# Optimization experiments

Measured on AMD Instinct MI355X. Metric: run time of the kernel, lower is better.

Reference implementation:

```python
import jax, jax.numpy as jnp
import numpy as np

N = 50000      # nodes
E = 800000     # edges
T = 3          # npass
ED = 64        # embedding_dim
NS = 23        # nshifts (arange(0.8, 3.0+1e-5, 0.1))
MD = NS + ED   # message_dim = 87
H = 200        # hidden width (hardcoded in module)
NMOL = 2048    # number of molecules (segments for final scatter)
RD = ED * (T + 1)  # readout input dim = 256
EPS = 1e-5

SHIFTS = jnp.asarray(np.arange(0.8, 3.0 + 1e-5, 0.1, dtype=np.float32))  # [23]


def setup_inputs() -> dict:
    key = jax.random.key(0)
    ks = jax.random.split(key, 32)
    inp = {
        'z_i': jax.random.randint(ks[0], (N,), 0, 10),
        'edge_index': jax.random.randint(ks[1], (2, E), 0, N),
        'dist_ij': jax.random.uniform(ks[2], (E, 1), dtype=jnp.float32) * 2.2 + 0.8,
        'mol_ind': jnp.sort(jax.random.randint(ks[3], (N,), 0, NMOL)),
        'emb': jax.random.normal(ks[4], (10, ED), dtype=jnp.float32),
        # per-pass update MLP params, stacked over T
        'up_bn_g': jnp.ones((T, MD), jnp.float32),
        'up_bn_b': jnp.zeros((T, MD), jnp.float32),
        'up_w1': jax.random.normal(ks[5], (T, MD, H), jnp.float32) * 0.05,
        'up_b1': jnp.zeros((T, H), jnp.float32),
        'up_w2': jax.random.normal(ks[6], (T, H, H), jnp.float32) * 0.05,
        'up_b2': jnp.zeros((T, H), jnp.float32),
        'up_w3': jax.random.normal(ks[7], (T, H, H), jnp.float32) * 0.05,
        'up_b3': jnp.zeros((T, H), jnp.float32),
        'up_w4': jax.random.normal(ks[8], (T, H, ED), jnp.float32) * 0.05,
        'up_b4': jnp.zeros((T, ED), jnp.float32),
        # readout MLP params
        'ro_bn_g': jnp.ones((RD,), jnp.float32),
        'ro_bn_b': jnp.zeros((RD,), jnp.float32),
        'ro_w1': jax.random.normal(ks[9], (RD, H), jnp.float32) * 0.05,
        'ro_b1': jnp.zeros((H,), jnp.float32),
        'ro_w2': jax.random.normal(ks[10], (H, H), jnp.float32) * 0.05,
        'ro_b2': jnp.zeros((H,), jnp.float32),
        'ro_w3': jax.random.normal(ks[11], (H, H), jnp.float32) * 0.05,
        'ro_b3': jnp.zeros((H,), jnp.float32),
        'ro_w4': jax.random.normal(ks[12], (H, 1), jnp.float32) * 0.05,
        'ro_b4': jnp.zeros((1,), jnp.float32),  # bias filled to 0 in __init__
    }
    return inp


def batchnorm(x, g, b):
    # BatchNorm1d in training mode: batch statistics, biased variance
    mu = jnp.mean(x, axis=0)
    var = jnp.mean(jnp.square(x - mu), axis=0)
    return (x - mu) * jax.lax.rsqrt(var + EPS) * g + b


def mlp(x, g, b, w1, b1, w2, b2, w3, b3, w4, b4):
    x = batchnorm(x, g, b)
    x = jax.nn.relu(x @ w1 + b1)
    x = jax.nn.relu(x @ w2 + b2)
    x = jax.nn.relu(x @ w3 + b3)
    return x @ w4 + b4


def reference(z_i, edge_index, dist_ij, mol_ind, emb,
              up_bn_g, up_bn_b, up_w1, up_b1, up_w2, up_b2, up_w3, up_b3, up_w4, up_b4,
              ro_bn_g, ro_bn_b, ro_w1, ro_b1, ro_w2, ro_b2, ro_w3, ro_b3, ro_w4, ro_b4):
    e_source, e_sink = edge_index[0], edge_index[1]
    rbf_ij = jnp.exp(-jnp.square(dist_ij - SHIFTS[None, :]))  # [E, NS]
    x_i = emb[z_i]                                            # [N, ED]
    x_list = [x_i]
    for t in range(T):
        m_ij = jnp.concatenate([rbf_ij, x_i[e_sink]], axis=1)  # [E, MD] gather
        m_i = jax.ops.segment_sum(m_ij, e_source, num_segments=N)  # scatter-sum
        x_i = x_i + 0.1 * mlp(m_i, up_bn_g[t], up_bn_b[t],
                              up_w1[t], up_b1[t], up_w2[t], up_b2[t],
                              up_w3[t], up_b3[t], up_w4[t], up_b4[t])
        x_list.append(x_i)
    x_all = jnp.concatenate(x_list, axis=1)  # [N, RD]
    y_i = mlp(x_all, ro_bn_g, ro_bn_b, ro_w1, ro_b1, ro_w2, ro_b2, ro_w3, ro_b3, ro_w4, ro_b4)
    y = jax.ops.segment_sum(y_i, mol_ind, num_segments=NMOL)  # [NMOL, 1]
    return y
```

## Files before the change

kernel.cpp:

```cpp
#include <hip/hip_runtime.h>
#include <hip/hip_bf16.h>
#include <type_traits>

#define NN 50000
#define NP 50048
#define EE 800000
#define TT 3
#define ED 64
#define NS 23
#define MD 87
#define HH 200
#define NMOL 2048
#define RD 256

#define SP 216
#define NPB2 512
#define SNB ((NN + 255) / 256)

typedef __attribute__((ext_vector_type(8))) short short8b;
typedef __attribute__((ext_vector_type(4))) short short4b;
typedef __attribute__((ext_vector_type(4))) float f32x4;

__device__ __forceinline__ unsigned short f2bf(float f) {
  unsigned u = __float_as_uint(f);
  return (unsigned short)((u + 0x7fffu + ((u >> 16) & 1u)) >> 16);
}
__device__ __forceinline__ float ubf2f(unsigned short h) {
  return __uint_as_float(((unsigned)h) << 16);
}
__device__ __forceinline__ float bfp2f(unsigned p) {
  return __uint_as_float(p << 16) + __uint_as_float(p & 0xffff0000u);
}
__device__ __forceinline__ unsigned packsplit(float v) {
  unsigned short h = f2bf(v);
  unsigned short l = f2bf(v - ubf2f(h));
  return (unsigned)h | ((unsigned)l << 16);
}

struct WD { const float* src; short* dst; int K, N, Kpad, Npad, T; };
struct WDs { WD d[5]; };

__global__ __launch_bounds__(256) void wprep_kernel(WDs W) {
  WD w = W.d[blockIdx.y];
  int KB = w.Kpad >> 5, NT = w.Npad >> 4;
  int per = w.Npad * w.Kpad;
  int total = w.T * per;
  for (int idx = blockIdx.x * 256 + threadIdx.x; idx < total; idx += gridDim.x * 256) {
    int t = idx / per;
    int r = idx - t * per;
    int e = r & 7, lane = (r >> 3) & 63;
    int blk = r >> 9;
    int kb = blk % KB, tile = blk / KB;
    int ln = lane & 15, quad = lane >> 4;
    int n = tile * 16 + ln, k = kb * 32 + quad * 8 + e;
    float v = 0.f;
    if (k < w.K && n < w.N) v = w.src[((size_t)t * w.K + k) * w.N + n];
    unsigned short h = f2bf(v);
    unsigned short l = f2bf(v - ubf2f(h));
    size_t base = ((size_t)(t * NT + tile) * KB + kb) * 1024;
    w.dst[base + lane * 8 + e] = (short)h;
    w.dst[base + 512 + lane * 8 + e] = (short)l;
  }
}

__global__ __launch_bounds__(256) void wscale_kernel(const float* __restrict__ wsrc,
                                                     const float* __restrict__ na,
                                                     const float* __restrict__ nb,
                                                     const float* __restrict__ bsrc,
                                                     int K, int Kpad,
                                                     short* __restrict__ wsp,
                                                     float* __restrict__ bc) {
  int n = blockIdx.x;
  int k = threadIdx.x;
  int KB = Kpad >> 5;
  int tile = n >> 4, ln = n & 15;
  float contrib = 0.f;
  if (k < Kpad) {
    float v = 0.f;
    if (n < HH && k < K) {
      float w = wsrc[(size_t)k * HH + n];
      v = na[k] * w;
      contrib = nb[k] * w;
    }
    unsigned short h = f2bf(v);
    unsigned short l = f2bf(v - ubf2f(h));
    int kb = k >> 5, quad = (k & 31) >> 3, e = k & 7;
    int lane = quad * 16 + ln;
    size_t base = ((size_t)tile * KB + kb) * 1024;
    wsp[base + lane * 8 + e] = (short)h;
    wsp[base + 512 + lane * 8 + e] = (short)l;
  }
  __shared__ float sh[256];
  sh[k] = contrib;
  __syncthreads();
  for (int off = 128; off > 0; off >>= 1) {
    if (k < off) sh[k] += sh[k + off];
    __syncthreads();
  }
  if (k == 0) bc[n] = (n < HH ? bsrc[n] : 0.f) + sh[0];
}

__global__ __launch_bounds__(256) void emb_kernel(const int* __restrict__ z,
                                                  const float* __restrict__ emb,
                                                  unsigned* __restrict__ xp,
                                                  short* __restrict__ xq) {
  int idx = blockIdx.x * 256 + threadIdx.x;
  if (idx >= NN * ED) return;
  int i = idx >> 6, d = idx & 63;
  unsigned pk = packsplit(emb[z[i] * ED + d]);
  xp[(size_t)i * RD + d] = pk;
  xq[(size_t)i * RD + d] = (short)(pk & 0xffffu);
}

__global__ __launch_bounds__(256) void hist_kernel(const int* __restrict__ src,
                                                   int* __restrict__ deg) {
  int e = blockIdx.x * 256 + threadIdx.x;
  if (e < EE) atomicAdd(&deg[src[e]], 1);
}

__global__ __launch_bounds__(256) void scanA_kernel(const int* __restrict__ deg,
                                                    int* __restrict__ Psum) {
  int i = blockIdx.x * 256 + threadIdx.x;
  int v = (i < NN) ? deg[i] : 0;
#pragma unroll
  for (int off = 32; off > 0; off >>= 1) v += __shfl_down(v, off, 64);
  __shared__ int ws[4];
  if ((threadIdx.x & 63) == 0) ws[threadIdx.x >> 6] = v;
  __syncthreads();
  if (threadIdx.x == 0) Psum[blockIdx.x] = ws[0] + ws[1] + ws[2] + ws[3];
}

__global__ __launch_bounds__(256) void scanB_kernel(const int* __restrict__ Psum,
                                                    int* __restrict__ Poff) {
  __shared__ int sh[256];
  int t = threadIdx.x;
  int v = (t < SNB) ? Psum[t] : 0;
  sh[t] = v;
  __syncthreads();
  for (int off = 1; off < 256; off <<= 1) {
    int u = (t >= off) ? sh[t - off] : 0;
    __syncthreads();
    sh[t] += u;
    __syncthreads();
  }
  if (t < SNB) Poff[t] = sh[t] - v;
}

__global__ __launch_bounds__(256) void scanC_kernel(const int* __restrict__ deg,
                                                    const int* __restrict__ Poff,
                                                    int* __restrict__ offs,
                                                    int* __restrict__ cursor) {
  __shared__ int sh[256];
  int t = threadIdx.x;
  int i = blockIdx.x * 256 + t;
  int v = (i < NN) ? deg[i] : 0;
  sh[t] = v;
  __syncthreads();
  for (int off = 1; off < 256; off <<= 1) {
    int u = (t >= off) ? sh[t - off] : 0;
    __syncthreads();
    sh[t] += u;
    __syncthreads();
  }
  int excl = Poff[blockIdx.x] + sh[t] - v;
  if (i < NN) {
    offs[i] = excl;
    cursor[i] = excl;
    if (i == NN - 1) offs[NN] = excl + v;
  }
}

__global__ __launch_bounds__(256) void scatter_kernel(const int* __restrict__ src,
                                                      const int* __restrict__ snk,
                                                      const float* __restrict__ dist,
                                                      int* __restrict__ cursor,
                                                      int* __restrict__ ssink,
                                                      float* __restrict__ sdist) {
  int e = blockIdx.x * 256 + threadIdx.x;
  if (e >= EE) return;
  int p = atomicAdd(&cursor[src[e]], 1);
  ssink[p] = snk[e];
  sdist[p] = dist[e];
}

__global__ __launch_bounds__(256) void gather_kernel(const int* __restrict__ offs,
                                                     const int* __restrict__ ssink,
                                                     const float* __restrict__ sdist,
                                                     const short* __restrict__ xq,
                                                     int toff, short* __restrict__ mh) {
  int node = blockIdx.x * 4 + (threadIdx.x >> 6);
  int lane = threadIdx.x & 63;
  if (node >= NN) return;
  float shift = (float)(0.8 + 0.1 * (double)lane);
  int e0 = offs[node], e1 = offs[node + 1];
  float ax0 = 0.f, ax1 = 0.f, ar0 = 0.f, ar1 = 0.f;
  int j = e0;
  for (; j + 4 <= e1; j += 4) {
    int s0 = ssink[j], s1 = ssink[j + 1], s2 = ssink[j + 2], s3 = ssink[j + 3];
    float d0 = sdist[j], d1 = sdist[j + 1], d2 = sdist[j + 2], d3 = sdist[j + 3];
    float x0 = ubf2f((unsigned short)xq[(size_t)s0 * RD + toff + lane]);
    float x1 = ubf2f((unsigned short)xq[(size_t)s1 * RD + toff + lane]);
    float x2 = ubf2f((unsigned short)xq[(size_t)s2 * RD + toff + lane]);
    float x3 = ubf2f((unsigned short)xq[(size_t)s3 * RD + toff + lane]);
    ax0 += x0 + x2;
    ax1 += x1 + x3;
    if (lane < NS) {
      float u0 = d0 - shift, u1 = d1 - shift, u2 = d2 - shift, u3 = d3 - shift;
      ar0 += __expf(-u0 * u0) + __expf(-u2 * u2);
      ar1 += __expf(-u1 * u1) + __expf(-u3 * u3);
    }
  }
  for (; j < e1; j++) {
    int s = ssink[j];
    float d = sdist[j];
    ax0 += ubf2f((unsigned short)xq[(size_t)s * RD + toff + lane]);
    if (lane < NS) {
      float u = d - shift;
      ar0 += __expf(-u * u);
    }
  }
  float accx = ax0 + ax1, accr = ar0 + ar1;
  if (lane < NS) mh[(size_t)node * 96 + lane] = (short)f2bf(accr);
  mh[(size_t)node * 96 + NS + lane] = (short)f2bf(accx);
}

template <int LD>
__global__ __launch_bounds__(256) void colstats_s16_kernel(const short* __restrict__ X,
                                                           float* __restrict__ P) {
  constexpr int CG = LD / 8;
  constexpr int RPB = 256 / CG;
  const int t = threadIdx.x;
  const int cg = t % CG, rin = t / CG;
  float s[8] = {0, 0, 0, 0, 0, 0, 0, 0}, q[8] = {0, 0, 0, 0, 0, 0, 0, 0};
  if (rin < RPB) {
    for (int r = blockIdx.x * RPB + rin; r < NN; r += gridDim.x * RPB) {
      union { uint4 v; short e[8]; } u;
      u.v = *(const uint4*)(X + (size_t)r * LD + cg * 8);
#pragma unroll
      for (int e = 0; e < 8; e++) {
        float f = ubf2f((unsigned short)u.e[e]);
        s[e] += f;
        q[e] += f * f;
      }
    }
  }
  __shared__ float sh[256][16];
#pragma unroll
  for (int e = 0; e < 8; e++) { sh[t][e] = s[e]; sh[t][8 + e] = q[e]; }
  __syncthreads();
  if (rin == 0) {
    for (int rr = 1; rr < RPB; rr++) {
      const float* o = sh[rr * CG + cg];
#pragma unroll
      for (int e = 0; e < 8; e++) { s[e] += o[e]; q[e] += o[8 + e]; }
    }
    float* Pb = P + blockIdx.x * 512;
#pragma unroll
    for (int e = 0; e < 8; e++) {
      Pb[cg * 8 + e] = s[e];
      Pb[256 + cg * 8 + e] = q[e];
    }
  }
}

__global__ __launch_bounds__(256) void bnfinal2_kernel(const float* __restrict__ P, int nblk,
                                                       const float* __restrict__ g,
                                                       const float* __restrict__ b, int ncols,
                                                       float* __restrict__ na,
                                                       float* __restrict__ nb) {
  int c = blockIdx.x;
  int t = threadIdx.x;
  float s = 0.f, q = 0.f;
  for (int i = t; i < nblk; i += 256) {
    s += P[i * 512 + c];
    q += P[i * 512 + 256 + c];
  }
#pragma unroll
  for (int off = 32; off > 0; off >>= 1) {
    s += __shfl_down(s, off, 64);
    q += __shfl_down(q, off, 64);
  }
  __shared__ float ws[4], wq[4];
  if ((t & 63) == 0) { ws[t >> 6] = s; wq[t >> 6] = q; }
  __syncthreads();
  if (t == 0) {
    s = ws[0] + ws[1] + ws[2] + ws[3];
    q = wq[0] + wq[1] + wq[2] + wq[3];
    if (c < ncols) {
      float mean = s / (float)NN;
      float var = q / (float)NN - mean * mean;
      float a = g[c] * rsqrtf(var + 1e-5f);
      na[c] = a;
      nb[c] = b[c] - mean * a;
    } else {
      na[c] = 0.f;
      nb[c] = 0.f;
    }
  }
}

template <bool READOUT>
__global__ __launch_bounds__(512, 4) void fused_kernel(
    const short* __restrict__ Agh, int glda,
    const short* __restrict__ W1p, int KB1,
    const short* __restrict__ W2p, const short* __restrict__ W3p,
    const short* __restrict__ W4p,
    const float* __restrict__ b1, const float* __restrict__ b2,
    const float* __restrict__ b3, const float* __restrict__ b4,
    unsigned* __restrict__ xp, short* __restrict__ xq, int t,
    const float* __restrict__ w4ro, const int* __restrict__ mol,
    float* __restrict__ out) {
  __shared__ short ldsH[64 * SP + 16];
  const int tid = threadIdx.x;
  const int wave = tid >> 6, lane = tid & 63, ln = lane & 15, quad = lane >> 4;
  const int bm = blockIdx.x * 64;
  const int ntile = (wave < 5) ? 2 : 1;
  const int tile0 = (wave < 5) ? 2 * wave : wave + 5;
  const int n0col = tile0 * 16;

  if (tid < 16) ldsH[64 * SP + tid] = 0;

  f32x4 acc[4][2];

  auto layer = [&](auto ga_tag, auto terms_tag, const short* __restrict__ Wp,
                   int KB, int KP) {
    constexpr bool GA = decltype(ga_tag)::value;
    constexpr int TERMS = decltype(terms_tag)::value;
#pragma unroll
    for (int i = 0; i < 4; i++)
#pragma unroll
      for (int j = 0; j < 2; j++) acc[i][j] = (f32x4){0.f, 0.f, 0.f, 0.f};
    for (int k0 = 0; k0 < KP; k0 += 32) {
      const int kb = k0 >> 5;
      short8b ah[4], bh[2], bl[2];
#pragma unroll
      for (int i = 0; i < 4; i++) {
        int r = i * 16 + ln;
        if constexpr (GA)
          ah[i] = *(const short8b*)(Agh + (size_t)(bm + r) * glda + k0 + quad * 8);
        else
          ah[i] = *(const short8b*)(ldsH + r * SP + k0 + quad * 8);
      }
#pragma unroll
      for (int j = 0; j < 2; j++)
        if (j < ntile) {
          const short* bp = Wp + ((size_t)((tile0 + j) * KB + kb)) * 1024 + lane * 8;
          bh[j] = *(const short8b*)bp;
          if constexpr (TERMS == 2) bl[j] = *(const short8b*)(bp + 512);
        }
#pragma unroll
      for (int j = 0; j < 2; j++)
        if (j < ntile)
#pragma unroll
          for (int i = 0; i < 4; i++) {
            acc[i][j] = __builtin_amdgcn_mfma_f32_16x16x32_bf16(ah[i], bh[j], acc[i][j], 0, 0, 0);
            if constexpr (TERMS == 2)
              acc[i][j] =
                  __builtin_amdgcn_mfma_f32_16x16x32_bf16(ah[i], bl[j], acc[i][j], 0, 0, 0);
          }
    }
  };

  auto epi = [&](const float* __restrict__ bias) {
    __syncthreads();
#pragma unroll
    for (int i = 0; i < 4; i++)
#pragma unroll
      for (int j = 0; j < 2; j++)
        if (j < ntile)
#pragma unroll
          for (int r = 0; r < 4; r++) {
            int row = i * 16 + quad * 4 + r;
            int col = n0col + j * 16 + ln;
            float v = acc[i][j][r] + (col < HH ? bias[col] : 0.f);
            v = fmaxf(v, 0.f);
            ldsH[row * SP + col] = (short)f2bf(v);
          }
    ldsH[(tid >> 3) * SP + 208 + (tid & 7)] = 0;
    __syncthreads();
  };

  using one_t = std::integral_constant<int, 1>;
  using two_t = std::integral_constant<int, 2>;

  if (!READOUT) {
    layer(std::true_type{}, two_t{}, W1p, KB1, 96);
    epi(b1);
    layer(std::false_type{}, one_t{}, W2p, 7, 224);
    epi(b2);
    layer(std::false_type{}, one_t{}, W3p, 7, 224);
    epi(b3);
    const int wm4 = wave & 1, wn4 = wave >> 1;
    f32x4 a4[2];
#pragma unroll
    for (int i = 0; i < 2; i++) a4[i] = (f32x4){0.f, 0.f, 0.f, 0.f};
    for (int k0 = 0; k0 < 224; k0 += 32) {
      const int kb = k0 >> 5;
      short8b ah[2], bh, bl;
#pragma unroll
      for (int i = 0; i < 2; i++) {
        int r = wm4 * 32 + i * 16 + ln;
        ah[i] = *(const short8b*)(ldsH + r * SP + k0 + quad * 8);
      }
      const short* bp = W4p + ((size_t)(wn4 * 7 + kb)) * 1024 + lane * 8;
      bh = *(const short8b*)bp;
      bl = *(const short8b*)(bp + 512);
#pragma unroll
      for (int i = 0; i < 2; i++) {
        a4[i] = __builtin_amdgcn_mfma_f32_16x16x32_bf16(ah[i], bh, a4[i], 0, 0, 0);
        a4[i] = __builtin_amdgcn_mfma_f32_16x16x32_bf16(ah[i], bl, a4[i], 0, 0, 0);
      }
    }
#pragma unroll
    for (int i = 0; i < 2; i++)
#pragma unroll
      for (int r = 0; r < 4; r++) {
        int grow = bm + wm4 * 32 + i * 16 + quad * 4 + r;
        int col = wn4 * 16 + ln;
        if (grow < NN) {
          float v = a4[i][r] + b4[col];
          size_t base = (size_t)grow * RD;
          float old = bfp2f(xp[base + (size_t)t * ED + col]);
          unsigned pk = packsplit(old + 0.1f * v);
          xp[base + (size_t)(t + 1) * ED + col] = pk;
          xq[base + (size_t)(t + 1) * ED + col] = (short)(pk & 0xffffu);
        }
      }
  } else {
    layer(std::true_type{}, two_t{}, W1p, KB1, 256);
    epi(b1);
    layer(std::false_type{}, one_t{}, W2p, 7, 224);
    epi(b2);
    layer(std::false_type{}, one_t{}, W3p, 7, 224);
    epi(b3);
    int row = tid >> 3;
    int grow = bm + row;
    float s = 0.f;
    for (int c = (tid & 7); c < HH; c += 8)
      s += ubf2f((unsigned short)ldsH[row * SP + c]) * w4ro[c];
    s += __shfl_xor(s, 1, 64);
    s += __shfl_xor(s, 2, 64);
    s += __shfl_xor(s, 4, 64);
    if ((tid & 7) == 0 && grow < NN) atomicAdd(&out[mol[grow]], s + b4[0]);
  }
}

extern "C" void kernel_launch(void* const* d_in, const int* in_sizes, int n_in,
                              void* d_out, int out_size, void* d_ws, size_t ws_size,
                              hipStream_t stream) {
  const int* z_i = (const int*)d_in[0];
  const int* e_src = (const int*)d_in[1];
  const int* e_snk = ((const int*)d_in[1]) + EE;
  const float* dist = (const float*)d_in[2];
  const int* mol = (const int*)d_in[3];
  const float* emb = (const float*)d_in[4];
  const float* up_bn_g = (const float*)d_in[5];
  const float* up_bn_b = (const float*)d_in[6];
  const float* up_w1 = (const float*)d_in[7];
  const float* up_b1 = (const float*)d_in[8];
  const float* up_w2 = (const float*)d_in[9];
  const float* up_b2 = (const float*)d_in[10];
  const float* up_w3 = (const float*)d_in[11];
  const float* up_b3 = (const float*)d_in[12];
  const float* up_w4 = (const float*)d_in[13];
  const float* up_b4 = (const float*)d_in[14];
  const float* ro_bn_g = (const float*)d_in[15];
  const float* ro_bn_b = (const float*)d_in[16];
  const float* ro_w1 = (const float*)d_in[17];
  const float* ro_b1 = (const float*)d_in[18];
  const float* ro_w2 = (const float*)d_in[19];
  const float* ro_b2 = (const float*)d_in[20];
  const float* ro_w3 = (const float*)d_in[21];
  const float* ro_b3 = (const float*)d_in[22];
  const float* ro_w4 = (const float*)d_in[23];
  const float* ro_b4 = (const float*)d_in[24];
  float* out = (float*)d_out;

  char* p = (char*)d_ws;
  auto alloc = [&](size_t bytes) {
    void* r = (void*)p;
    p += (bytes + 255) & ~(size_t)255;
    return r;
  };
  unsigned* x_p = (unsigned*)alloc((size_t)NN * RD * 4);
  short* x_q = (short*)alloc((size_t)NP * RD * 2);
  short* mh = (short*)alloc((size_t)NP * 96 * 2);
  int* ssink = (int*)alloc((size_t)EE * 4);
  float* sdist = (float*)alloc((size_t)EE * 4);
  int* offs = (int*)alloc((size_t)(NN + 1) * 4);
  int* deg = (int*)alloc((size_t)NN * 4);
  int* cursor = (int*)alloc((size_t)NN * 4);
  int* Psum = (int*)alloc((size_t)SNB * 4);
  int* Poff = (int*)alloc((size_t)SNB * 4);
  float* P = (float*)alloc((size_t)NPB2 * 512 * 4);
  float* na = (float*)alloc(256 * 4);
  float* nb = (float*)alloc(256 * 4);
  float* b1c = (float*)alloc(208 * 4);
  short* w1sp = (short*)alloc((size_t)13 * 3 * 1024 * 2);
  short* r1sp = (short*)alloc((size_t)13 * 8 * 1024 * 2);
  short* w2p = (short*)alloc((size_t)TT * 13 * 7 * 1024 * 2);
  short* w3p = (short*)alloc((size_t)TT * 13 * 7 * 1024 * 2);
  short* w4p = (short*)alloc((size_t)TT * 4 * 7 * 1024 * 2);
  short* r2p = (short*)alloc((size_t)13 * 7 * 1024 * 2);
  short* r3p = (short*)alloc((size_t)13 * 7 * 1024 * 2);

  hipMemsetAsync(deg, 0, (size_t)NN * 4, stream);
  hipMemsetAsync(out, 0, (size_t)NMOL * 4, stream);

  WDs descs;
  descs.d[0] = {up_w2, w2p, HH, HH, 224, 208, TT};
  descs.d[1] = {up_w3, w3p, HH, HH, 224, 208, TT};
  descs.d[2] = {up_w4, w4p, HH, ED, 224, 64, TT};
  descs.d[3] = {ro_w2, r2p, HH, HH, 224, 208, 1};
  descs.d[4] = {ro_w3, r3p, HH, HH, 224, 208, 1};
  wprep_kernel<<<dim3(546, 5), 256, 0, stream>>>(descs);

  emb_kernel<<<(NN * ED + 255) / 256, 256, 0, stream>>>(z_i, emb, x_p, x_q);
  hist_kernel<<<(EE + 255) / 256, 256, 0, stream>>>(e_src, deg);
  scanA_kernel<<<SNB, 256, 0, stream>>>(deg, Psum);
  scanB_kernel<<<1, 256, 0, stream>>>(Psum, Poff);
  scanC_kernel<<<SNB, 256, 0, stream>>>(deg, Poff, offs, cursor);
  scatter_kernel<<<(EE + 255) / 256, 256, 0, stream>>>(e_src, e_snk, dist, cursor, ssink, sdist);

  const int gM = NP / 64;

  for (int t = 0; t < TT; t++) {
    gather_kernel<<<(NN + 3) / 4, 256, 0, stream>>>(offs, ssink, sdist, x_q, t * ED, mh);
    colstats_s16_kernel<96><<<NPB2, 256, 0, stream>>>(mh, P);
    bnfinal2_kernel<<<256, 256, 0, stream>>>(P, NPB2, up_bn_g + t * MD, up_bn_b + t * MD, MD,
                                             na, nb);
    wscale_kernel<<<208, 256, 0, stream>>>(up_w1 + (size_t)t * MD * HH, na, nb,
                                           up_b1 + t * HH, MD, 96, w1sp, b1c);
    fused_kernel<false><<<gM, 512, 0, stream>>>(
        mh, 96, w1sp, 3,
        w2p + (size_t)t * 13 * 7 * 1024, w3p + (size_t)t * 13 * 7 * 1024,
        w4p + (size_t)t * 4 * 7 * 1024,
        b1c, up_b2 + t * HH, up_b3 + t * HH, up_b4 + t * ED,
        x_p, x_q, t, nullptr, nullptr, nullptr);
  }

  colstats_s16_kernel<256><<<NPB2, 256, 0, stream>>>(x_q, P);
  bnfinal2_kernel<<<256, 256, 0, stream>>>(P, NPB2, ro_bn_g, ro_bn_b, RD, na, nb);
  wscale_kernel<<<208, 256, 0, stream>>>(ro_w1, na, nb, ro_b1, RD, 256, r1sp, b1c);
  fused_kernel<true><<<gM, 512, 0, stream>>>(
      x_q, 256, r1sp, 8,
      r2p, r3p, nullptr,
      b1c, ro_b2, ro_b3, ro_b4,
      nullptr, nullptr, 0, ro_w4, mol, out);

  (void)in_sizes; (void)n_in; (void)out_size; (void)ws_size;
}
```

Before: 613.2 us.

## Compact per-pass gather buffer and compute RBF sums only in first pass

Adds a separate dense [T+1, N, 64] bf16 copy of the node features, written by the embedding and fused update kernels. The edge gather reads this copy instead of the strided 256-wide x_q rows. The gather kernel is templated so that the radial-basis sums, which do not change between passes, are computed and stored into mh only in pass 0. Passes 1 and 2 reuse those mh columns and skip the dist loads and exp evaluations. The cost is extra global writes for the duplicated features, plus reliance on mh's RBF columns not being overwritten between passes.

Result: faster. 593.4 us (-3.2%).

```diff
diff --git a/kernel.cpp b/kernel.cpp
--- a/kernel.cpp
+++ b/kernel.cpp
@@ -103,13 +103,16 @@
 __global__ __launch_bounds__(256) void emb_kernel(const int* __restrict__ z,
                                                   const float* __restrict__ emb,
                                                   unsigned* __restrict__ xp,
-                                                  short* __restrict__ xq) {
+                                                  short* __restrict__ xq,
+                                                  short* __restrict__ xqs) {
   int idx = blockIdx.x * 256 + threadIdx.x;
   if (idx >= NN * ED) return;
   int i = idx >> 6, d = idx & 63;
   unsigned pk = packsplit(emb[z[i] * ED + d]);
   xp[(size_t)i * RD + d] = pk;
-  xq[(size_t)i * RD + d] = (short)(pk & 0xffffu);
+  short h = (short)(pk & 0xffffu);
+  xq[(size_t)i * RD + d] = h;
+  xqs[(size_t)i * ED + d] = h;
 }
 
 __global__ __launch_bounds__(256) void hist_kernel(const int* __restrict__ src,
@@ -183,11 +186,12 @@
   sdist[p] = dist[e];
 }
 
+template <bool RBF>
 __global__ __launch_bounds__(256) void gather_kernel(const int* __restrict__ offs,
                                                      const int* __restrict__ ssink,
                                                      const float* __restrict__ sdist,
-                                                     const short* __restrict__ xq,
-                                                     int toff, short* __restrict__ mh) {
+                                                     const short* __restrict__ xqs,
+                                                     short* __restrict__ mh) {
   int node = blockIdx.x * 4 + (threadIdx.x >> 6);
   int lane = threadIdx.x & 63;
   if (node >= NN) return;
@@ -197,14 +201,14 @@
   int j = e0;
   for (; j + 4 <= e1; j += 4) {
     int s0 = ssink[j], s1 = ssink[j + 1], s2 = ssink[j + 2], s3 = ssink[j + 3];
-    float d0 = sdist[j], d1 = sdist[j + 1], d2 = sdist[j + 2], d3 = sdist[j + 3];
-    float x0 = ubf2f((unsigned short)xq[(size_t)s0 * RD + toff + lane]);
-    float x1 = ubf2f((unsigned short)xq[(size_t)s1 * RD + toff + lane]);
-    float x2 = ubf2f((unsigned short)xq[(size_t)s2 * RD + toff + lane]);
-    float x3 = ubf2f((unsigned short)xq[(size_t)s3 * RD + toff + lane]);
+    float x0 = ubf2f((unsigned short)xqs[(size_t)s0 * ED + lane]);
+    float x1 = ubf2f((unsigned short)xqs[(size_t)s1 * ED + lane]);
+    float x2 = ubf2f((unsigned short)xqs[(size_t)s2 * ED + lane]);
+    float x3 = ubf2f((unsigned short)xqs[(size_t)s3 * ED + lane]);
     ax0 += x0 + x2;
     ax1 += x1 + x3;
-    if (lane < NS) {
+    if (RBF && lane < NS) {
+      float d0 = sdist[j], d1 = sdist[j + 1], d2 = sdist[j + 2], d3 = sdist[j + 3];
       float u0 = d0 - shift, u1 = d1 - shift, u2 = d2 - shift, u3 = d3 - shift;
       ar0 += __expf(-u0 * u0) + __expf(-u2 * u2);
       ar1 += __expf(-u1 * u1) + __expf(-u3 * u3);
@@ -212,15 +216,14 @@
   }
   for (; j < e1; j++) {
     int s = ssink[j];
-    float d = sdist[j];
-    ax0 += ubf2f((unsigned short)xq[(size_t)s * RD + toff + lane]);
-    if (lane < NS) {
-      float u = d - shift;
+    ax0 += ubf2f((unsigned short)xqs[(size_t)s * ED + lane]);
+    if (RBF && lane < NS) {
+      float u = sdist[j] - shift;
       ar0 += __expf(-u * u);
     }
   }
-  float accx = ax0 + ax1, accr = ar0 + ar1;
-  if (lane < NS) mh[(size_t)node * 96 + lane] = (short)f2bf(accr);
+  float accx = ax0 + ax1;
+  if (RBF && lane < NS) mh[(size_t)node * 96 + lane] = (short)f2bf(ar0 + ar1);
   mh[(size_t)node * 96 + NS + lane] = (short)f2bf(accx);
 }
 
@@ -307,8 +310,8 @@
     const short* __restrict__ W4p,
     const float* __restrict__ b1, const float* __restrict__ b2,
     const float* __restrict__ b3, const float* __restrict__ b4,
-    unsigned* __restrict__ xp, short* __restrict__ xq, int t,
-    const float* __restrict__ w4ro, const int* __restrict__ mol,
+    unsigned* __restrict__ xp, short* __restrict__ xq, short* __restrict__ xqs,
+    int t, const float* __restrict__ w4ro, const int* __restrict__ mol,
     float* __restrict__ out) {
   __shared__ short ldsH[64 * SP + 16];
   const int tid = threadIdx.x;
@@ -423,7 +426,9 @@
           float old = bfp2f(xp[base + (size_t)t * ED + col]);
           unsigned pk = packsplit(old + 0.1f * v);
           xp[base + (size_t)(t + 1) * ED + col] = pk;
-          xq[base + (size_t)(t + 1) * ED + col] = (short)(pk & 0xffffu);
+          short h = (short)(pk & 0xffffu);
+          xq[base + (size_t)(t + 1) * ED + col] = h;
+          xqs[(size_t)(t + 1) * NN * ED + (size_t)grow * ED + col] = h;
         }
       }
   } else {
@@ -484,6 +489,7 @@
   };
   unsigned* x_p = (unsigned*)alloc((size_t)NN * RD * 4);
   short* x_q = (short*)alloc((size_t)NP * RD * 2);
+  short* x_qs = (short*)alloc((size_t)(TT + 1) * NN * ED * 2);
   short* mh = (short*)alloc((size_t)NP * 96 * 2);
   int* ssink = (int*)alloc((size_t)EE * 4);
   float* sdist = (float*)alloc((size_t)EE * 4);
@@ -515,7 +521,7 @@
   descs.d[4] = {ro_w3, r3p, HH, HH, 224, 208, 1};
   wprep_kernel<<<dim3(546, 5), 256, 0, stream>>>(descs);
 
-  emb_kernel<<<(NN * ED + 255) / 256, 256, 0, stream>>>(z_i, emb, x_p, x_q);
+  emb_kernel<<<(NN * ED + 255) / 256, 256, 0, stream>>>(z_i, emb, x_p, x_q, x_qs);
   hist_kernel<<<(EE + 255) / 256, 256, 0, stream>>>(e_src, deg);
   scanA_kernel<<<SNB, 256, 0, stream>>>(deg, Psum);
   scanB_kernel<<<1, 256, 0, stream>>>(Psum, Poff);
@@ -525,7 +531,12 @@
   const int gM = NP / 64;
 
   for (int t = 0; t < TT; t++) {
-    gather_kernel<<<(NN + 3) / 4, 256, 0, stream>>>(offs, ssink, sdist, x_q, t * ED, mh);
+    if (t == 0)
+      gather_kernel<true><<<(NN + 3) / 4, 256, 0, stream>>>(
+          offs, ssink, sdist, x_qs, mh);
+    else
+      gather_kernel<false><<<(NN + 3) / 4, 256, 0, stream>>>(
+          offs, ssink, sdist, x_qs + (size_t)t * NN * ED, mh);
     colstats_s16_kernel<96><<<NPB2, 256, 0, stream>>>(mh, P);
     bnfinal2_kernel<<<256, 256, 0, stream>>>(P, NPB2, up_bn_g + t * MD, up_bn_b + t * MD, MD,
                                              na, nb);
@@ -536,7 +547,7 @@
         w2p + (size_t)t * 13 * 7 * 1024, w3p + (size_t)t * 13 * 7 * 1024,
         w4p + (size_t)t * 4 * 7 * 1024,
         b1c, up_b2 + t * HH, up_b3 + t * HH, up_b4 + t * ED,
-        x_p, x_q, t, nullptr, nullptr, nullptr);
+        x_p, x_q, x_qs, t, nullptr, nullptr, nullptr);
   }
 
   colstats_s16_kernel<256><<<NPB2, 256, 0, stream>>>(x_q, P);
@@ -546,7 +557,7 @@
       x_q, 256, r1sp, 8,
       r2p, r3p, nullptr,
       b1c, ro_b2, ro_b3, ro_b4,
-      nullptr, nullptr, 0, ro_w4, mol, out);
+      nullptr, nullptr, nullptr, 0, ro_w4, mol, out);
 
   (void)in_sizes; (void)n_in; (void)out_size; (void)ws_size;
 }
```
